# Optimization experiments

Measured on AMD Instinct MI355X. Metric: run time of the kernel, lower is better.

Reference implementation:

```python
import jax, jax.numpy as jnp
import numpy as np

H, D, EPS = 4, 16, 1e-5
N_NODES, N_EDGES, F_IN, HID, N_GRAPHS, N_CLASSES = 100000, 1600000, 128, 64, 512, 10


def _bn(x, g, b, m, v):
    # BatchNorm1d in eval mode: running stats
    return (x - m) * jax.lax.rsqrt(v + EPS) * g + b


def _tconv(x, src, dst, wq, bq, wk, bk, wv, bv, ws, bs):
    # PyG TransformerConv: q from dst node, k/v from src node, scatter-softmax over dst,
    # scatter-add aggregation, concat heads, plus root (skip) linear. Dropout=eval (identity).
    N = x.shape[0]
    q = (x @ wq + bq).reshape(N, H, D)
    k = (x @ wk + bk).reshape(N, H, D)
    v = (x @ wv + bv).reshape(N, H, D)
    alpha = (q[dst] * k[src]).sum(-1) * np.float32(1.0 / np.sqrt(D))  # [E, H]
    amax = jax.ops.segment_max(alpha, dst, num_segments=N)            # [N, H]
    amax = jnp.where(jnp.isfinite(amax), amax, 0.0)
    ex = jnp.exp(alpha - amax[dst])
    denom = jax.ops.segment_sum(ex, dst, num_segments=N)
    attn = ex / (denom[dst] + 1e-16)                                  # [E, H]
    agg = jax.ops.segment_sum(attn[:, :, None] * v[src], dst, num_segments=N)  # [N, H, D]
    return agg.reshape(N, H * D) + x @ ws + bs


def setup_inputs() -> dict:
    key = jax.random.key(0)
    ks = list(jax.random.split(key, 40))
    def w(i, shape):
        return jax.random.normal(ks[i], shape, jnp.float32) * 0.05
    inp = {}
    inp['x'] = jax.random.normal(ks[0], (N_NODES, F_IN), jnp.float32)
    inp['edge_index'] = jax.random.randint(ks[1], (2, N_EDGES), 0, N_NODES, dtype=jnp.int32)
    inp['batch'] = jnp.sort(jax.random.randint(ks[2], (N_NODES,), 0, N_GRAPHS, dtype=jnp.int32))
    i = 3
    for p, fin in (('c1', F_IN), ('c2', HID)):
        for nm in ('wq', 'wk', 'wv', 'ws'):
            inp[p + '_' + nm] = w(i, (fin, HID)); i += 1
            inp[p + '_b' + nm[1]] = w(i, (HID,)); i += 1
    for p in ('bn1', 'bn2', 'clbn'):
        inp[p + '_g'] = jnp.ones((HID,), jnp.float32)
        inp[p + '_b'] = jnp.zeros((HID,), jnp.float32)
        inp[p + '_m'] = jnp.zeros((HID,), jnp.float32)
        inp[p + '_v'] = jnp.ones((HID,), jnp.float32)
    for nm, shp in (('p1_w', (HID, HID)), ('p2_w', (HID, HID)), ('cl1_w', (HID, HID)), ('cl2_w', (HID, N_CLASSES))):
        inp[nm] = w(i, shp); i += 1
    inp['p1_b'] = jnp.zeros((HID,), jnp.float32)
    inp['p2_b'] = jnp.zeros((HID,), jnp.float32)
    inp['cl1_b'] = jnp.zeros((HID,), jnp.float32)
    inp['cl2_b'] = jnp.zeros((N_CLASSES,), jnp.float32)
    return inp


def reference(x, edge_index, batch,
              c1_wq, c1_bq, c1_wk, c1_bk, c1_wv, c1_bv, c1_ws, c1_bs,
              bn1_g, bn1_b, bn1_m, bn1_v,
              c2_wq, c2_bq, c2_wk, c2_bk, c2_wv, c2_bv, c2_ws, c2_bs,
              bn2_g, bn2_b, bn2_m, bn2_v,
              p1_w, p1_b, p2_w, p2_b,
              cl1_w, cl1_b, clbn_g, clbn_b, clbn_m, clbn_v, cl2_w, cl2_b):
    src, dst = edge_index[0], edge_index[1]
    h = _tconv(x, src, dst, c1_wq, c1_bq, c1_wk, c1_bk, c1_wv, c1_bv, c1_ws, c1_bs)
    h = jax.nn.relu(_bn(h, bn1_g, bn1_b, bn1_m, bn1_v))
    h = _tconv(h, src, dst, c2_wq, c2_bq, c2_wk, c2_bk, c2_wv, c2_bv, c2_ws, c2_bs)
    h = jax.nn.relu(_bn(h, bn2_g, bn2_b, bn2_m, bn2_v))
    g = jax.ops.segment_max(h, batch, num_segments=N_GRAPHS)  # global_max_pool [G, HID]
    g = jnp.where(jnp.isfinite(g), g, 0.0)
    g = jax.nn.relu(g @ p1_w + p1_b) @ p2_w + p2_b
    g = jax.nn.relu(_bn(g @ cl1_w + cl1_b, clbn_g, clbn_b, clbn_m, clbn_v))
    logits = g @ cl2_w + cl2_b
    return jax.nn.log_softmax(logits, axis=1)
```

## Files before the change

kernel.cpp:

```cpp
#include <hip/hip_runtime.h>
#include <hip/hip_bf16.h>
#include <math.h>

constexpr int NN = 100000;
constexpr int EE = 1600000;
constexpr int GG = 512;
constexpr int MPAD = 100096;
constexpr int NBUCK = 782;
constexpr int EPB = 8192;

typedef __attribute__((ext_vector_type(8))) short short8;
typedef __attribute__((ext_vector_type(4))) float floatx4;

__device__ __forceinline__ unsigned short f2bf_rne(float f) {
    unsigned int u = __float_as_uint(f);
    u += 0x7fff + ((u >> 16) & 1);
    return (unsigned short)(u >> 16);
}

template<int C>
__device__ __forceinline__ float dppadd(float x) {
    int t = __builtin_amdgcn_update_dpp(0, __float_as_int(x), C, 0xf, 0xf, true);
    return x + __int_as_float(t);
}
__device__ __forceinline__ float hred16(float p) {
    p = dppadd<0xB1>(p);
    p = dppadd<0x4E>(p);
    p = dppadd<0x124>(p);
    p = dppadd<0x128>(p);
    return p;
}

__global__ __launch_bounds__(512) void k_bhist(const int* __restrict__ dst,
                                               int* __restrict__ bcnt) {
    __shared__ int cnt[NBUCK];
    int tid = threadIdx.x;
    int e0 = blockIdx.x * EPB;
    for (int j = tid; j < NBUCK; j += 512) cnt[j] = 0;
    __syncthreads();
    #pragma unroll
    for (int t = 0; t < 16; t++) {
        int i = e0 + t * 512 + tid;
        if (i < EE) atomicAdd(&cnt[dst[i] >> 7], 1);
    }
    __syncthreads();
    for (int j = tid; j < NBUCK; j += 512) if (cnt[j]) atomicAdd(&bcnt[j], cnt[j]);
}

__global__ __launch_bounds__(1024) void k_bscan(const int* __restrict__ bcnt,
                                                int* __restrict__ bbase,
                                                int* __restrict__ bcur) {
    __shared__ int sa[1024], sb[1024];
    int t = threadIdx.x;
    sa[t] = (t < NBUCK) ? bcnt[t] : 0;
    __syncthreads();
    int* p = sa; int* q = sb;
    for (int off = 1; off < 1024; off <<= 1) {
        q[t] = (t >= off) ? (p[t] + p[t - off]) : p[t];
        __syncthreads();
        int* tmp = p; p = q; q = tmp;
    }
    int excl = (t == 0) ? 0 : p[t - 1];
    if (t < NBUCK) { bbase[t] = excl; bcur[t] = excl; }
    if (t == NBUCK - 1) bbase[NBUCK] = p[NBUCK - 1];
}

__global__ __launch_bounds__(512) void k_part(const int* __restrict__ src,
                                              const int* __restrict__ dst,
                                              int* __restrict__ bcur,
                                              int2* __restrict__ ppair) {
    __shared__ int cnt[NBUCK];
    __shared__ int base[NBUCK];
    int tid = threadIdx.x;
    int e0 = blockIdx.x * EPB;
    for (int j = tid; j < NBUCK; j += 512) cnt[j] = 0;
    __syncthreads();
    int myd[16], myr[16];
    #pragma unroll
    for (int t = 0; t < 16; t++) {
        int i = e0 + t * 512 + tid;
        if (i < EE) {
            int d = dst[i];
            myd[t] = d;
            myr[t] = atomicAdd(&cnt[d >> 7], 1);
        } else myd[t] = -1;
    }
    __syncthreads();
    for (int j = tid; j < NBUCK; j += 512) base[j] = atomicAdd(&bcur[j], cnt[j]);
    __syncthreads();
    #pragma unroll
    for (int t = 0; t < 16; t++) {
        int i = e0 + t * 512 + tid;
        if (myd[t] >= 0) {
            int2 pr; pr.x = src[i]; pr.y = myd[t];
            ppair[base[myd[t] >> 7] + myr[t]] = pr;
        }
    }
}

__global__ __launch_bounds__(256) void k_bucket(const int2* __restrict__ ppair,
                                                const int* __restrict__ bbase,
                                                int* __restrict__ rowp,
                                                int* __restrict__ csr) {
    __shared__ int cnt[128];
    __shared__ int sa[128], sb[128];
    __shared__ int cur[128];
    int t = threadIdx.x;
    int b = blockIdx.x;
    int start = bbase[b], end = bbase[b + 1];
    if (t < 128) cnt[t] = 0;
    __syncthreads();
    for (int i = start + t; i < end; i += 256)
        atomicAdd(&cnt[ppair[i].y & 127], 1);
    __syncthreads();
    if (t < 128) sa[t] = cnt[t];
    __syncthreads();
    int* p = sa; int* q = sb;
    for (int off = 1; off < 128; off <<= 1) {
        if (t < 128) q[t] = (t >= off) ? (p[t] + p[t - off]) : p[t];
        __syncthreads();
        int* tmp = p; p = q; q = tmp;
    }
    if (t < 128) {
        int excl = (t == 0) ? 0 : p[t - 1];
        rowp[b * 128 + t] = start + excl;
        cur[t] = start + excl;
    }
    __syncthreads();
    for (int i = start + t; i < end; i += 256) {
        int2 e = ppair[i];
        int pos = atomicAdd(&cur[e.y & 127], 1);
        csr[pos] = e.x;
    }
}

template<int K>
__global__ __launch_bounds__(256) void k_cvt_w(
    const float* __restrict__ Wq, const float* __restrict__ Bq,
    const float* __restrict__ Wk, const float* __restrict__ Bk,
    const float* __restrict__ Wv, const float* __restrict__ Bv,
    const float* __restrict__ Wsk, const float* __restrict__ Bsk,
    unsigned short* __restrict__ Bt, float* __restrict__ bias) {
    int idx = blockIdx.x * 256 + threadIdx.x;
    int col = idx / K, k = idx % K;
    float val;
    if (col < 128) {
        int f = col >> 1;
        val = (col & 1) ? Wv[k * 64 + f] : Wk[k * 64 + f];
    } else if (col < 192) {
        val = Wq[k * 64 + (col - 128)];
    } else {
        val = Wsk[k * 64 + (col - 192)];
    }
    Bt[col * K + k] = f2bf_rne(val);
    if (k == 0) {
        float bv;
        if (col < 128) {
            int f = col >> 1;
            bv = (col & 1) ? Bv[f] : Bk[f];
        } else if (col < 192) bv = Bq[col - 128];
        else bv = Bsk[col - 192];
        bias[col] = bv;
    }
}

template<int K, bool AF32>
__global__ __launch_bounds__(256) void gemm_mfma(
    const void* __restrict__ Araw,
    const unsigned short* __restrict__ Bt,
    const float* __restrict__ bias,
    float* __restrict__ qs,
    unsigned short* __restrict__ kvu) {
    constexpr int SP = 72;
    __shared__ short As[128 * SP];
    __shared__ short Bs[128 * SP];
    int tid = threadIdx.x;
    int wave = tid >> 6, lane = tid & 63;
    int wm = wave >> 1, wn = wave & 1;
    int quad = lane >> 4, l16 = lane & 15;
    int rowBase = blockIdx.x * 128;
    int ct = blockIdx.y;

    floatx4 acc[4][4];
    #pragma unroll
    for (int i = 0; i < 4; i++)
        #pragma unroll
        for (int j = 0; j < 4; j++) acc[i][j] = (floatx4)0.f;

    for (int kc = 0; kc < K; kc += 64) {
        #pragma unroll
        for (int it = 0; it < 4; it++) {
            int flat = it * 256 + tid;
            int r = flat >> 3, c8 = (flat & 7) * 8;
            int ar = rowBase + r; if (ar >= NN) ar = NN - 1;
            short8 va;
            if constexpr (AF32) {
                const float* ap = (const float*)Araw + (size_t)ar * K + kc + c8;
                float4 u0 = *reinterpret_cast<const float4*>(ap);
                float4 u1 = *reinterpret_cast<const float4*>(ap + 4);
                va[0] = (short)f2bf_rne(u0.x); va[1] = (short)f2bf_rne(u0.y);
                va[2] = (short)f2bf_rne(u0.z); va[3] = (short)f2bf_rne(u0.w);
                va[4] = (short)f2bf_rne(u1.x); va[5] = (short)f2bf_rne(u1.y);
                va[6] = (short)f2bf_rne(u1.z); va[7] = (short)f2bf_rne(u1.w);
            } else {
                va = *reinterpret_cast<const short8*>(
                        (const unsigned short*)Araw + (size_t)ar * K + kc + c8);
            }
            *reinterpret_cast<short8*>(&As[r * SP + c8]) = va;
            short8 vb = *reinterpret_cast<const short8*>(Bt + (size_t)(ct * 128 + r) * K + kc + c8);
            *reinterpret_cast<short8*>(&Bs[r * SP + c8]) = vb;
        }
        __syncthreads();
        #pragma unroll
        for (int ks = 0; ks < 2; ks++) {
            short8 af[4], bf[4];
            #pragma unroll
            for (int i = 0; i < 4; i++)
                af[i] = *reinterpret_cast<const short8*>(&As[(wm * 64 + i * 16 + l16) * SP + ks * 32 + quad * 8]);
            #pragma unroll
            for (int j = 0; j < 4; j++)
                bf[j] = *reinterpret_cast<const short8*>(&Bs[(wn * 64 + j * 16 + l16) * SP + ks * 32 + quad * 8]);
            #pragma unroll
            for (int i = 0; i < 4; i++)
                #pragma unroll
                for (int j = 0; j < 4; j++)
                    acc[i][j] = __builtin_amdgcn_mfma_f32_16x16x32_bf16(af[i], bf[j], acc[i][j], 0, 0, 0);
        }
        __syncthreads();
    }

    float bj[4];
    #pragma unroll
    for (int j = 0; j < 4; j++) bj[j] = bias[ct * 128 + wn * 64 + j * 16 + l16];
    #pragma unroll
    for (int i = 0; i < 4; i++) {
        #pragma unroll
        for (int j = 0; j < 4; j++) {
            int col = wn * 64 + j * 16 + l16;
            #pragma unroll
            for (int r = 0; r < 4; r++) {
                int row = rowBase + wm * 64 + i * 16 + quad * 4 + r;
                if (row < NN) {
                    float val = acc[i][j][r] + bj[j];
                    if (ct == 1) qs[(size_t)row * 128 + col] = val;
                    else kvu[(size_t)row * 128 + col] = f2bf_rne(val);
                }
            }
        }
    }
}

__global__ __launch_bounds__(256) void attn_fused(
    const float* __restrict__ qs,
    const unsigned int* __restrict__ kv,
    const int* __restrict__ row_ptr,
    const int* __restrict__ csr_src,
    const float* __restrict__ bng, const float* __restrict__ bnb,
    const float* __restrict__ bnm, const float* __restrict__ bnv,
    unsigned short* __restrict__ h_out) {
    int wid = (blockIdx.x * 256 + threadIdx.x) >> 6;
    int lane = threadIdx.x & 63;
    if (wid >= NN) return;
    float q = qs[(size_t)wid * 128 + lane] * 0.3606737602222409f;
    float skip = qs[(size_t)wid * 128 + 64 + lane];
    int jb = row_ptr[wid], je = row_ptr[wid + 1];
    float acc = 0.f, denom = 0.f;
    int j = jb;
    for (; j + 3 < je; j += 4) {
        int s0 = csr_src[j], s1 = csr_src[j + 1];
        int s2 = csr_src[j + 2], s3 = csr_src[j + 3];
        unsigned int c0 = kv[(size_t)s0 * 64 + lane];
        unsigned int c1 = kv[(size_t)s1 * 64 + lane];
        unsigned int c2 = kv[(size_t)s2 * 64 + lane];
        unsigned int c3 = kv[(size_t)s3 * 64 + lane];
        float k0 = __uint_as_float(c0 << 16), v0 = __uint_as_float(c0 & 0xffff0000u);
        float k1 = __uint_as_float(c1 << 16), v1 = __uint_as_float(c1 & 0xffff0000u);
        float k2 = __uint_as_float(c2 << 16), v2 = __uint_as_float(c2 & 0xffff0000u);
        float k3 = __uint_as_float(c3 << 16), v3 = __uint_as_float(c3 & 0xffff0000u);
        float p0 = hred16(q * k0);
        float p1 = hred16(q * k1);
        float p2 = hred16(q * k2);
        float p3 = hred16(q * k3);
        float e0 = exp2f(p0), e1 = exp2f(p1), e2 = exp2f(p2), e3 = exp2f(p3);
        denom += (e0 + e1) + (e2 + e3);
        acc = fmaf(e0, v0, acc);
        acc = fmaf(e1, v1, acc);
        acc = fmaf(e2, v2, acc);
        acc = fmaf(e3, v3, acc);
    }
    for (; j < je; j++) {
        int s0 = csr_src[j];
        unsigned int c0 = kv[(size_t)s0 * 64 + lane];
        float k0 = __uint_as_float(c0 << 16), v0 = __uint_as_float(c0 & 0xffff0000u);
        float e0 = exp2f(hred16(q * k0));
        denom += e0;
        acc = fmaf(e0, v0, acc);
    }
    float o = acc / (denom + 1e-16f) + skip;
    o = (o - bnm[lane]) * rsqrtf(bnv[lane] + 1e-5f) * bng[lane] + bnb[lane];
    h_out[(size_t)wid * 64 + lane] = f2bf_rne(fmaxf(o, 0.f));
}

__global__ __launch_bounds__(256) void k_pool(const unsigned short* __restrict__ h,
                                              const int* __restrict__ batch,
                                              float* __restrict__ g0) {
    int f = threadIdx.x & 63;
    int sub = threadIdx.x >> 6;
    int n0 = blockIdx.x * 128;
    int nEnd = n0 + 128; if (nEnd > NN) nEnd = NN;
    int cur_g = -1; float cur_m = 0.f;
    for (int n = n0 + sub; n < nEnd; n += 4) {
        int bg = batch[n];
        float val = __uint_as_float((unsigned int)h[(size_t)n * 64 + f] << 16);
        if (bg != cur_g) {
            if (cur_g >= 0) atomicMax((int*)&g0[cur_g * 64 + f], __float_as_int(cur_m));
            cur_g = bg; cur_m = val;
        } else {
            cur_m = fmaxf(cur_m, val);
        }
    }
    if (cur_g >= 0) atomicMax((int*)&g0[cur_g * 64 + f], __float_as_int(cur_m));
}

__global__ __launch_bounds__(256) void k_mlp(
    const float* __restrict__ g0,
    const float* __restrict__ p1w, const float* __restrict__ p1b,
    const float* __restrict__ p2w, const float* __restrict__ p2b,
    const float* __restrict__ cl1w, const float* __restrict__ cl1b,
    const float* __restrict__ bg, const float* __restrict__ bb,
    const float* __restrict__ bm, const float* __restrict__ bv,
    const float* __restrict__ cl2w, const float* __restrict__ cl2b,
    float* __restrict__ outp) {
    __shared__ float w1[64 * 64], w2[64 * 64], w3[64 * 64], w4[64 * 10];
    __shared__ float sb1[64], sb2[64], sb3[64], sbn[4 * 64], sb4[10];
    int tid = threadIdx.x;
    for (int i = tid; i < 64 * 64; i += 256) { w1[i] = p1w[i]; w2[i] = p2w[i]; w3[i] = cl1w[i]; }
    for (int i = tid; i < 64 * 10; i += 256) w4[i] = cl2w[i];
    if (tid < 64) {
        sb1[tid] = p1b[tid]; sb2[tid] = p2b[tid]; sb3[tid] = cl1b[tid];
        sbn[tid] = bg[tid]; sbn[64 + tid] = bb[tid];
        sbn[128 + tid] = bm[tid]; sbn[192 + tid] = bv[tid];
    }
    if (tid < 10) sb4[tid] = cl2b[tid];
    __syncthreads();
    int lane = tid & 63, w = tid >> 6;
    int row = blockIdx.x * 4 + w;
    float x = g0[row * 64 + lane];
    if (!isfinite(x)) x = 0.f;
    float a = sb1[lane];
    for (int k = 0; k < 64; k++) a += __shfl(x, k) * w1[k * 64 + lane];
    x = fmaxf(a, 0.f);
    a = sb2[lane];
    for (int k = 0; k < 64; k++) a += __shfl(x, k) * w2[k * 64 + lane];
    x = a;
    a = sb3[lane];
    for (int k = 0; k < 64; k++) a += __shfl(x, k) * w3[k * 64 + lane];
    a = (a - sbn[128 + lane]) * rsqrtf(sbn[192 + lane] + 1e-5f) * sbn[lane] + sbn[64 + lane];
    x = fmaxf(a, 0.f);
    float lg[10];
    #pragma unroll
    for (int c = 0; c < 10; c++) {
        float p = x * w4[lane * 10 + c];
        p += __shfl_xor(p, 1);  p += __shfl_xor(p, 2);  p += __shfl_xor(p, 4);
        p += __shfl_xor(p, 8);  p += __shfl_xor(p, 16); p += __shfl_xor(p, 32);
        lg[c] = p + sb4[c];
    }
    float mx = lg[0];
    #pragma unroll
    for (int c = 1; c < 10; c++) mx = fmaxf(mx, lg[c]);
    float s = 0.f;
    #pragma unroll
    for (int c = 0; c < 10; c++) s += __expf(lg[c] - mx);
    float lse = mx + logf(s);
    float o = 0.f;
    #pragma unroll
    for (int c = 0; c < 10; c++) if (lane == c) o = lg[c];
    if (lane < 10) outp[row * 10 + lane] = o - lse;
}

extern "C" void kernel_launch(void* const* d_in, const int* in_sizes, int n_in,
                              void* d_out, int out_size, void* d_ws, size_t ws_size,
                              hipStream_t stream) {
    const float* x     = (const float*)d_in[0];
    const int*   ei    = (const int*)d_in[1];
    const int*   batch = (const int*)d_in[2];
    const float *c1_wq = (const float*)d_in[3],  *c1_bq = (const float*)d_in[4];
    const float *c1_wk = (const float*)d_in[5],  *c1_bk = (const float*)d_in[6];
    const float *c1_wv = (const float*)d_in[7],  *c1_bv = (const float*)d_in[8];
    const float *c1_ws = (const float*)d_in[9],  *c1_bs = (const float*)d_in[10];
    const float *c2_wq = (const float*)d_in[11], *c2_bq = (const float*)d_in[12];
    const float *c2_wk = (const float*)d_in[13], *c2_bk = (const float*)d_in[14];
    const float *c2_wv = (const float*)d_in[15], *c2_bv = (const float*)d_in[16];
    const float *c2_ws = (const float*)d_in[17], *c2_bs = (const float*)d_in[18];
    const float *bn1_g = (const float*)d_in[19], *bn1_b = (const float*)d_in[20];
    const float *bn1_m = (const float*)d_in[21], *bn1_v = (const float*)d_in[22];
    const float *bn2_g = (const float*)d_in[23], *bn2_b = (const float*)d_in[24];
    const float *bn2_m = (const float*)d_in[25], *bn2_v = (const float*)d_in[26];
    const float *clbn_g = (const float*)d_in[27], *clbn_b = (const float*)d_in[28];
    const float *clbn_m = (const float*)d_in[29], *clbn_v = (const float*)d_in[30];
    const float *p1_w = (const float*)d_in[31], *p2_w = (const float*)d_in[32];
    const float *cl1_w = (const float*)d_in[33], *cl2_w = (const float*)d_in[34];
    const float *p1_b = (const float*)d_in[35], *p2_b = (const float*)d_in[36];
    const float *cl1_b = (const float*)d_in[37], *cl2_b = (const float*)d_in[38];

    char* ws = (char*)d_ws;
    float*          qs    = (float*)(ws);
    unsigned int*   kv    = (unsigned int*)(ws + 51200000);
    unsigned short* hbuf  = (unsigned short*)(ws + 76800000);
    int2*           ppair = (int2*)(ws + 89612288);
    int*            csr   = (int*)(ws + 102412288);
    int*            rowp  = (int*)(ws + 108812288);
    int*            bcnt  = (int*)(ws + 109212688);
    int*            bbase = (int*)(ws + 109215824);
    int*            bcur  = (int*)(ws + 109218960);
    float*          g0    = (float*)(ws + 109222096);
    unsigned short* Bt1   = (unsigned short*)(ws + 109353168);
    float*          b1    = (float*)(ws + 109418704);
    unsigned short* Bt2   = (unsigned short*)(ws + 109419728);
    float*          b2    = (float*)(ws + 109452496);

    const int* srcIdx = ei;
    const int* dstIdx = ei + EE;

    hipMemsetAsync(bcnt, 0, NBUCK * sizeof(int), stream);
    hipMemsetAsync(g0, 0, GG * 64 * sizeof(float), stream);

    constexpr int PBLK = (EE + EPB - 1) / EPB;
    k_bhist<<<PBLK, 512, 0, stream>>>(dstIdx, bcnt);
    k_bscan<<<1, 1024, 0, stream>>>(bcnt, bbase, bcur);
    k_part<<<PBLK, 512, 0, stream>>>(srcIdx, dstIdx, bcur, ppair);
    k_bucket<<<NBUCK, 256, 0, stream>>>(ppair, bbase, rowp, csr);

    k_cvt_w<128><<<128, 256, 0, stream>>>(c1_wq, c1_bq, c1_wk, c1_bk, c1_wv, c1_bv,
                                          c1_ws, c1_bs, Bt1, b1);
    k_cvt_w<64><<<64, 256, 0, stream>>>(c2_wq, c2_bq, c2_wk, c2_bk, c2_wv, c2_bv,
                                        c2_ws, c2_bs, Bt2, b2);

    {
        dim3 grid(MPAD / 128, 2);
        gemm_mfma<128, true><<<grid, 256, 0, stream>>>(x, Bt1, b1, qs, (unsigned short*)kv);
    }
    attn_fused<<<NN / 4, 256, 0, stream>>>(qs, kv, rowp, csr, bn1_g, bn1_b, bn1_m, bn1_v, hbuf);

    {
        dim3 grid(MPAD / 128, 2);
        gemm_mfma<64, false><<<grid, 256, 0, stream>>>(hbuf, Bt2, b2, qs, (unsigned short*)kv);
    }
    attn_fused<<<NN / 4, 256, 0, stream>>>(qs, kv, rowp, csr, bn2_g, bn2_b, bn2_m, bn2_v, hbuf);

    k_pool<<<(NN + 127) / 128, 256, 0, stream>>>(hbuf, batch, g0);
    k_mlp<<<GG / 4, 256, 0, stream>>>(g0, p1_w, p1_b, p2_w, p2_b, cl1_w, cl1_b,
                                      clbn_g, clbn_b, clbn_m, clbn_v, cl2_w, cl2_b,
                                      (float*)d_out);
}
```

Measured before the change: 452.8 us.

## Split KV layout and process two edges per wave in attention

Changes the projected K/V layout from interleaved k/v pairs to separate contiguous K and V halves per node. The attention kernel then has each half-wave handle a different edge, with each lane holding two features, and the two halves are combined by a cross-half shuffle at the end. The head reduction shrinks from a 16-lane to an 8-lane DPP sum, and the output is packed as bf16 pairs. The aim is to halve the per-edge instruction and latency chain and the reduction cost, at the price of more complex tail handling and a final cross-half reduction.

```diff
diff --git a/kernel.cpp b/kernel.cpp
--- a/kernel.cpp
+++ b/kernel.cpp
@@ -23,11 +23,10 @@
     int t = __builtin_amdgcn_update_dpp(0, __float_as_int(x), C, 0xf, 0xf, true);
     return x + __int_as_float(t);
 }
-__device__ __forceinline__ float hred16(float p) {
+__device__ __forceinline__ float hred8(float p) {
     p = dppadd<0xB1>(p);
     p = dppadd<0x4E>(p);
-    p = dppadd<0x124>(p);
-    p = dppadd<0x128>(p);
+    p = dppadd<0x141>(p);
     return p;
 }
 
@@ -144,22 +143,17 @@
     int idx = blockIdx.x * 256 + threadIdx.x;
     int col = idx / K, k = idx % K;
     float val;
-    if (col < 128) {
-        int f = col >> 1;
-        val = (col & 1) ? Wv[k * 64 + f] : Wk[k * 64 + f];
-    } else if (col < 192) {
-        val = Wq[k * 64 + (col - 128)];
-    } else {
-        val = Wsk[k * 64 + (col - 192)];
-    }
+    if (col < 64)        val = Wk[k * 64 + col];
+    else if (col < 128)  val = Wv[k * 64 + (col - 64)];
+    else if (col < 192)  val = Wq[k * 64 + (col - 128)];
+    else                 val = Wsk[k * 64 + (col - 192)];
     Bt[col * K + k] = f2bf_rne(val);
     if (k == 0) {
         float bv;
-        if (col < 128) {
-            int f = col >> 1;
-            bv = (col & 1) ? Bv[f] : Bk[f];
-        } else if (col < 192) bv = Bq[col - 128];
-        else bv = Bsk[col - 192];
+        if (col < 64)        bv = Bk[col];
+        else if (col < 128)  bv = Bv[col - 64];
+        else if (col < 192)  bv = Bq[col - 128];
+        else                 bv = Bsk[col - 192];
         bias[col] = bv;
     }
 }
@@ -252,53 +246,82 @@
 
 __global__ __launch_bounds__(256) void attn_fused(
     const float* __restrict__ qs,
-    const unsigned int* __restrict__ kv,
+    const unsigned int* __restrict__ kvp,
     const int* __restrict__ row_ptr,
     const int* __restrict__ csr_src,
     const float* __restrict__ bng, const float* __restrict__ bnb,
     const float* __restrict__ bnm, const float* __restrict__ bnv,
-    unsigned short* __restrict__ h_out) {
+    unsigned int* __restrict__ h_out) {
     int wid = (blockIdx.x * 256 + threadIdx.x) >> 6;
     int lane = threadIdx.x & 63;
     if (wid >= NN) return;
-    float q = qs[(size_t)wid * 128 + lane] * 0.3606737602222409f;
-    float skip = qs[(size_t)wid * 128 + 64 + lane];
+    int half = lane >> 5, sl = lane & 31;
+    const float* qrow = qs + (size_t)wid * 128;
+    float2 q2 = reinterpret_cast<const float2*>(qrow)[sl];
+    float q0 = q2.x * 0.3606737602222409f;
+    float q1 = q2.y * 0.3606737602222409f;
     int jb = row_ptr[wid], je = row_ptr[wid + 1];
-    float acc = 0.f, denom = 0.f;
+    float acc0 = 0.f, acc1 = 0.f, denom = 0.f;
     int j = jb;
     for (; j + 3 < je; j += 4) {
-        int s0 = csr_src[j], s1 = csr_src[j + 1];
-        int s2 = csr_src[j + 2], s3 = csr_src[j + 3];
-        unsigned int c0 = kv[(size_t)s0 * 64 + lane];
-        unsigned int c1 = kv[(size_t)s1 * 64 + lane];
-        unsigned int c2 = kv[(size_t)s2 * 64 + lane];
-        unsigned int c3 = kv[(size_t)s3 * 64 + lane];
-        float k0 = __uint_as_float(c0 << 16), v0 = __uint_as_float(c0 & 0xffff0000u);
-        float k1 = __uint_as_float(c1 << 16), v1 = __uint_as_float(c1 & 0xffff0000u);
-        float k2 = __uint_as_float(c2 << 16), v2 = __uint_as_float(c2 & 0xffff0000u);
-        float k3 = __uint_as_float(c3 << 16), v3 = __uint_as_float(c3 & 0xffff0000u);
-        float p0 = hred16(q * k0);
-        float p1 = hred16(q * k1);
-        float p2 = hred16(q * k2);
-        float p3 = hred16(q * k3);
-        float e0 = exp2f(p0), e1 = exp2f(p1), e2 = exp2f(p2), e3 = exp2f(p3);
-        denom += (e0 + e1) + (e2 + e3);
-        acc = fmaf(e0, v0, acc);
-        acc = fmaf(e1, v1, acc);
-        acc = fmaf(e2, v2, acc);
-        acc = fmaf(e3, v3, acc);
-    }
-    for (; j < je; j++) {
-        int s0 = csr_src[j];
-        unsigned int c0 = kv[(size_t)s0 * 64 + lane];
-        float k0 = __uint_as_float(c0 << 16), v0 = __uint_as_float(c0 & 0xffff0000u);
-        float e0 = exp2f(hred16(q * k0));
-        denom += e0;
-        acc = fmaf(e0, v0, acc);
-    }
-    float o = acc / (denom + 1e-16f) + skip;
-    o = (o - bnm[lane]) * rsqrtf(bnv[lane] + 1e-5f) * bng[lane] + bnb[lane];
-    h_out[(size_t)wid * 64 + lane] = f2bf_rne(fmaxf(o, 0.f));
+        int sA = csr_src[j + half];
+        int sB = csr_src[j + 2 + half];
+        const unsigned int* rA = kvp + (size_t)sA * 64;
+        const unsigned int* rB = kvp + (size_t)sB * 64;
+        unsigned int kdA = rA[sl], vdA = rA[32 + sl];
+        unsigned int kdB = rB[sl], vdB = rB[32 + sl];
+        float kA0 = __uint_as_float(kdA << 16), kA1 = __uint_as_float(kdA & 0xffff0000u);
+        float kB0 = __uint_as_float(kdB << 16), kB1 = __uint_as_float(kdB & 0xffff0000u);
+        float pA = fmaf(kA0, q0, kA1 * q1);
+        float pB = fmaf(kB0, q0, kB1 * q1);
+        pA = hred8(pA); pB = hred8(pB);
+        float eA = exp2f(pA), eB = exp2f(pB);
+        float vA0 = __uint_as_float(vdA << 16), vA1 = __uint_as_float(vdA & 0xffff0000u);
+        float vB0 = __uint_as_float(vdB << 16), vB1 = __uint_as_float(vdB & 0xffff0000u);
+        denom += eA + eB;
+        acc0 = fmaf(eA, vA0, acc0); acc1 = fmaf(eA, vA1, acc1);
+        acc0 = fmaf(eB, vB0, acc0); acc1 = fmaf(eB, vB1, acc1);
+    }
+    for (; j + 1 < je; j += 2) {
+        int s = csr_src[j + half];
+        const unsigned int* r = kvp + (size_t)s * 64;
+        unsigned int kd = r[sl], vd = r[32 + sl];
+        float k0 = __uint_as_float(kd << 16), k1 = __uint_as_float(kd & 0xffff0000u);
+        float p = hred8(fmaf(k0, q0, k1 * q1));
+        float e = exp2f(p);
+        float v0 = __uint_as_float(vd << 16), v1 = __uint_as_float(vd & 0xffff0000u);
+        denom += e;
+        acc0 = fmaf(e, v0, acc0); acc1 = fmaf(e, v1, acc1);
+    }
+    if (j < je) {
+        int s = csr_src[j];
+        const unsigned int* r = kvp + (size_t)s * 64;
+        unsigned int kd = r[sl], vd = r[32 + sl];
+        float k0 = __uint_as_float(kd << 16), k1 = __uint_as_float(kd & 0xffff0000u);
+        float p = hred8(fmaf(k0, q0, k1 * q1));
+        float e = (half == 0) ? exp2f(p) : 0.f;
+        float v0 = __uint_as_float(vd << 16), v1 = __uint_as_float(vd & 0xffff0000u);
+        denom += e;
+        acc0 = fmaf(e, v0, acc0); acc1 = fmaf(e, v1, acc1);
+    }
+    acc0 += __shfl_xor(acc0, 32);
+    acc1 += __shfl_xor(acc1, 32);
+    denom += __shfl_xor(denom, 32);
+    float inv = 1.f / (denom + 1e-16f);
+    float2 s2 = reinterpret_cast<const float2*>(qrow + 64)[sl];
+    float2 m2 = reinterpret_cast<const float2*>(bnm)[sl];
+    float2 v2 = reinterpret_cast<const float2*>(bnv)[sl];
+    float2 g2 = reinterpret_cast<const float2*>(bng)[sl];
+    float2 b2 = reinterpret_cast<const float2*>(bnb)[sl];
+    float o0 = acc0 * inv + s2.x;
+    float o1 = acc1 * inv + s2.y;
+    o0 = (o0 - m2.x) * rsqrtf(v2.x + 1e-5f) * g2.x + b2.x;
+    o1 = (o1 - m2.y) * rsqrtf(v2.y + 1e-5f) * g2.y + b2.y;
+    o0 = fmaxf(o0, 0.f); o1 = fmaxf(o1, 0.f);
+    if (half == 0) {
+        unsigned int hw = (unsigned int)f2bf_rne(o0) | ((unsigned int)f2bf_rne(o1) << 16);
+        h_out[(size_t)wid * 32 + sl] = hw;
+    }
 }
 
 __global__ __launch_bounds__(256) void k_pool(const unsigned short* __restrict__ h,
@@ -440,13 +463,15 @@
         dim3 grid(MPAD / 128, 2);
         gemm_mfma<128, true><<<grid, 256, 0, stream>>>(x, Bt1, b1, qs, (unsigned short*)kv);
     }
-    attn_fused<<<NN / 4, 256, 0, stream>>>(qs, kv, rowp, csr, bn1_g, bn1_b, bn1_m, bn1_v, hbuf);
+    attn_fused<<<NN / 4, 256, 0, stream>>>(qs, kv, rowp, csr, bn1_g, bn1_b, bn1_m, bn1_v,
+                                           (unsigned int*)hbuf);
 
     {
         dim3 grid(MPAD / 128, 2);
         gemm_mfma<64, false><<<grid, 256, 0, stream>>>(hbuf, Bt2, b2, qs, (unsigned short*)kv);
     }
-    attn_fused<<<NN / 4, 256, 0, stream>>>(qs, kv, rowp, csr, bn2_g, bn2_b, bn2_m, bn2_v, hbuf);
+    attn_fused<<<NN / 4, 256, 0, stream>>>(qs, kv, rowp, csr, bn2_g, bn2_b, bn2_m, bn2_v,
+                                           (unsigned int*)hbuf);
 
     k_pool<<<(NN + 127) / 128, 256, 0, stream>>>(hbuf, batch, g0);
     k_mlp<<<GG / 4, 256, 0, stream>>>(g0, p1_w, p1_b, p2_w, p2_b, cl1_w, cl1_b,
```

New measurement: 451.7 us. About the same (-0.2%).
